# Performance work log

Measured on AMD Instinct MI355X. Metric: run time of the kernel, lower is better.

## Reference

```python
import jax, jax.numpy as jnp
import numpy as np
from jax import lax

T = 8
TAU = 2.0
ALPHA = 4.0   # spikingjelly surrogate.Sigmoid default alpha
EPS = 1e-5


def _kaiming(key, shape, fan_in):
    return jax.random.normal(key, shape, jnp.float32) * np.sqrt(2.0 / fan_in)


def setup_inputs() -> dict:
    key = jax.random.key(0)
    ks = jax.random.split(key, 16)
    d = {}
    d['x'] = jax.random.normal(ks[0], (128, 3, 32, 32), jnp.float32)
    convs = [('1', 32, 3), ('2', 32, 32), ('3', 64, 32), ('4', 64, 64), ('5', 128, 64), ('6', 128, 128)]
    for i, (s, co, ci) in enumerate(convs):
        d['w' + s] = _kaiming(ks[1 + i], (co, ci, 3, 3), ci * 9)
        d['b' + s] = jnp.zeros((co,), jnp.float32)
        d['g' + s] = jnp.ones((co,), jnp.float32)
        d['be' + s] = jnp.zeros((co,), jnp.float32)
    d['fc1_w'] = _kaiming(ks[7], (128, 2048), 2048)
    d['fc1_b'] = jnp.zeros((128,), jnp.float32)
    d['fc2_w'] = _kaiming(ks[8], (10, 128), 128)
    d['fc2_b'] = jnp.zeros((10,), jnp.float32)
    return d


def _conv2d(x, w, b):  # x [M,C,H,W], w [O,I,3,3], pad=1 stride=1
    y = lax.conv_general_dilated(x, w, (1, 1), ((1, 1), (1, 1)),
                                 dimension_numbers=('NCHW', 'OIHW', 'NCHW'))
    return y + b[None, :, None, None]


def _bn(x, g, be):  # training-mode BN over merged (T*N,H,W) batch
    m = x.mean(axis=(0, 2, 3))
    v = x.var(axis=(0, 2, 3))
    inv = g / jnp.sqrt(v + EPS)
    return x * inv[None, :, None, None] + (be - m * inv)[None, :, None, None]


def _lif(x_seq, th):
    # spikingjelly LIFNode defaults: decay_input=True, v_reset=0 (hard reset),
    # surrogate sigmoid gradient. x_seq: [T, ...]
    def step(v, x):
        v = v + (x - v) / TAU
        sig = jax.nn.sigmoid(ALPHA * (v - th))
        hard = (v >= th).astype(x.dtype)
        spike = lax.stop_gradient(hard - sig) + sig  # fwd: heaviside, bwd: sigmoid'
        return v * (1.0 - spike), spike
    return lax.scan(step, jnp.zeros_like(x_seq[0]), x_seq)[1]


def _maxpool(x):  # [M,C,H,W] -> 2x2 stride 2
    return lax.reduce_window(x, -jnp.inf, lax.max, (1, 1, 2, 2), (1, 1, 2, 2), 'VALID')


def _cbl(xs, w, b, g, be, th):  # conv-bn over merged TN, LIF scan over T
    t, n = xs.shape[0], xs.shape[1]
    m = xs.reshape((t * n,) + xs.shape[2:])
    y = _bn(_conv2d(m, w, b), g, be)
    return _lif(y.reshape((t, n) + y.shape[1:]), th)


def _pool_seq(xs):
    t, n = xs.shape[0], xs.shape[1]
    y = _maxpool(xs.reshape((t * n,) + xs.shape[2:]))
    return y.reshape((t, n) + y.shape[1:])


def _forward(x, w1, b1, g1, be1, w2, b2, g2, be2, w3, b3, g3, be3,
             w4, b4, g4, be4, w5, b5, g5, be5, w6, b6, g6, be6,
             fc1_w, fc1_b, fc2_w, fc2_b):
    th = 1.0
    xs = jnp.broadcast_to(x[None], (T,) + x.shape)  # [T,N,3,32,32]
    xs = _cbl(xs, w1, b1, g1, be1, th)
    xs = _cbl(xs, w2, b2, g2, be2, th)
    xs = _pool_seq(xs)                                # [T,N,32,16,16]
    xs = _cbl(xs, w3, b3, g3, be3, th)
    xs = _cbl(xs, w4, b4, g4, be4, th)
    xs = _pool_seq(xs)                                # [T,N,64,8,8]
    xs = _cbl(xs, w5, b5, g5, be5, th)
    xs = _cbl(xs, w6, b6, g6, be6, th)
    xs = _pool_seq(xs)                                # [T,N,128,4,4]
    t, n = xs.shape[0], xs.shape[1]
    f = xs.reshape(t, n, -1)                          # [T,N,2048]
    h = jnp.einsum('tnf,of->tno', f, fc1_w) + fc1_b
    h = _lif(h, 1.0)
    o = jnp.einsum('tnf,of->tno', h, fc2_w) + fc2_b
    o = _lif(o, 1.0)
    return o.mean(axis=0)                             # [N,10]


def reference(x, w1, b1, g1, be1, w2, b2, g2, be2, w3, b3, g3, be3,
              w4, b4, g4, be4, w5, b5, g5, be5, w6, b6, g6, be6,
              fc1_w, fc1_b, fc2_w, fc2_b):
    return _forward(x, w1, b1, g1, be1, w2, b2, g2, be2, w3, b3, g3, be3,
                    w4, b4, g4, be4, w5, b5, g5, be5, w6, b6, g6, be6,
                    fc1_w, fc1_b, fc2_w, fc2_b)
```

## Files before the change

### kernel.cpp

```cpp
#include <hip/hip_runtime.h>
#include <stdint.h>


#define T_STEPS 8
#define NBATCH 128

typedef __attribute__((ext_vector_type(8))) short short8;
typedef __attribute__((ext_vector_type(4))) float f32x4;

__device__ __forceinline__ uint16_t f2bf(float f) {
    uint32_t x = __float_as_uint(f);
    uint32_t r = x + 0x7FFFu + ((x >> 16) & 1u);
    return (uint16_t)(r >> 16);
}
__device__ __forceinline__ float bf2f(uint16_t h) {
    return __uint_as_float(((uint32_t)h) << 16);
}

__global__ void zero_kernel(float* p, int n) {
    int i = blockIdx.x * blockDim.x + threadIdx.x;
    if (i < n) p[i] = 0.0f;
}

__device__ __forceinline__ void tsplit(float v, uint16_t& h1, uint16_t& h2, uint16_t& h3) {
    h1 = f2bf(v);
    const float r1 = v - bf2f(h1);
    h2 = f2bf(r1);
    const float r2 = r1 - bf2f(h2);
    h3 = f2bf(r2);
}

__device__ __forceinline__ void prep_conv_one(const float* __restrict__ w,
                                              uint16_t* __restrict__ wp, int i, int CIN) {
    const int KC = CIN >> 5;
    const int sh = i % 9;
    const int ci = (i / 9) % CIN;
    const int co = i / (9 * CIN);
    uint16_t h1, h2, h3;
    tsplit(w[i], h1, h2, h3);
    uint16_t* base = wp + (size_t)((co >> 4) * KC + (ci >> 5)) * 14976
                        + sh * 1664 + (co & 15) * 104 + (ci & 31);
    base[0] = h1;
    base[32] = h2;
    base[64] = h3;
}

__device__ __forceinline__ void prep_fc1_one(const float* __restrict__ w,
                                             uint16_t* __restrict__ wp, int i) {
    const int kp = i & 2047;
    const int o = i >> 11;
    const int px = kp >> 7, c = kp & 127;
    uint16_t h1, h2, h3;
    tsplit(w[o * 2048 + c * 16 + px], h1, h2, h3);
    uint16_t* base = wp + (size_t)((o >> 4) * 64 + (kp >> 5)) * 1664
                        + (o & 15) * 104 + (kp & 31);
    base[0] = h1;
    base[32] = h2;
    base[64] = h3;
}

__global__ void prep_all_kernel(const float* __restrict__ W2, const float* __restrict__ W3,
                                const float* __restrict__ W4, const float* __restrict__ W5,
                                const float* __restrict__ W6, const float* __restrict__ F1,
                                uint16_t* __restrict__ P2, uint16_t* __restrict__ P3,
                                uint16_t* __restrict__ P4, uint16_t* __restrict__ P5,
                                uint16_t* __restrict__ P6, uint16_t* __restrict__ PF) {
    int i = blockIdx.x * blockDim.x + threadIdx.x;
    if (i < 9216) { prep_conv_one(W2, P2, i, 32); return; }
    i -= 9216;
    if (i < 18432) { prep_conv_one(W3, P3, i, 32); return; }
    i -= 18432;
    if (i < 36864) { prep_conv_one(W4, P4, i, 64); return; }
    i -= 36864;
    if (i < 73728) { prep_conv_one(W5, P5, i, 64); return; }
    i -= 73728;
    if (i < 147456) { prep_conv_one(W6, P6, i, 128); return; }
    i -= 147456;
    if (i < 262144) prep_fc1_one(F1, PF, i);
}

__global__ void border_all_kernel(uint8_t* S1, uint8_t* S2, uint8_t* S3,
                                  uint8_t* S4, uint8_t* S5, uint8_t* S6) {
    int i = blockIdx.x * blockDim.x + threadIdx.x;
    uint8_t* s;
    int C, HP, WPP;
    if (i < 1081344) { s = S1; C = 32; HP = 34; WPP = 34; }
    else if ((i -= 1081344) < 557056) { s = S2; C = 32; HP = 18; WPP = 18; }
    else if ((i -= 557056) < 1114112) { s = S3; C = 64; HP = 18; WPP = 18; }
    else if ((i -= 1114112) < 589824) { s = S4; C = 64; HP = 10; WPP = 10; }
    else if ((i -= 589824) < 1179648) { s = S5; C = 128; HP = 10; WPP = 10; }
    else if ((i -= 1179648) < 655360) { s = S6; C = 128; HP = 6; WPP = 6; }
    else return;
    const int C4 = C >> 2;
    const int NB = 2 * WPP + 2 * (HP - 2);
    const int c4 = i % C4;
    const int b = (i / C4) % NB;
    const int img = i / (C4 * NB);
    int py, px;
    if (b < WPP) { py = 0; px = b; }
    else if (b < 2 * WPP) { py = HP - 1; px = b - WPP; }
    else { const int r = b - 2 * WPP; py = 1 + (r >> 1); px = (r & 1) ? (WPP - 1) : 0; }
    *(uint32_t*)&s[(size_t)img * (HP * WPP * C) + (py * WPP + px) * C + 4 * c4] = 0u;
}

__global__ void conv3x3_kernel(const float* __restrict__ in,
                               const float* __restrict__ wgt,
                               const float* __restrict__ bias,
                               float* __restrict__ y,
                               float* __restrict__ ssum,
                               float* __restrict__ ssq,
                               int Cin, int H, int W) {
    const int m  = blockIdx.x;
    const int co = blockIdx.y;
    const int Cout = gridDim.y;
    const int HW = H * W;

    const float* wco = wgt + (size_t)co * Cin * 9;
    const float bv = bias[co];

    float lsum = 0.0f, lsq = 0.0f;

    for (int p = threadIdx.x; p < HW; p += blockDim.x) {
        const int hy = p / W;
        const int wx = p - hy * W;
        float acc = bv;
        for (int ci = 0; ci < Cin; ++ci) {
            const float* inc = in + ((size_t)m * Cin + ci) * HW;
            const float* wc = wco + ci * 9;
#pragma unroll
            for (int ky = 0; ky < 3; ++ky) {
                const int iy = hy + ky - 1;
                if (iy < 0 || iy >= H) continue;
#pragma unroll
                for (int kx = 0; kx < 3; ++kx) {
                    const int ix = wx + kx - 1;
                    if (ix < 0 || ix >= W) continue;
                    acc += inc[iy * W + ix] * wc[ky * 3 + kx];
                }
            }
        }
        y[((size_t)m * HW + p) * Cout + co] = acc;
        lsum += acc;
        lsq += acc * acc;
    }

    __shared__ float r1[256];
    __shared__ float r2[256];
    const int tid = threadIdx.x;
    r1[tid] = lsum;
    r2[tid] = lsq;
    __syncthreads();
    for (int s = blockDim.x >> 1; s > 0; s >>= 1) {
        if (tid < s) {
            r1[tid] += r1[tid + s];
            r2[tid] += r2[tid + s];
        }
        __syncthreads();
    }
    if (tid == 0) {
        atomicAdd(&ssum[co], r1[0]);
        atomicAdd(&ssq[co], r2[0]);
    }
}

template <int CIN, int COUT, int H, int W, int ROWS, int IMPB, int NCO, int KSPLIT>
__global__ __launch_bounds__(256) void conv_mfma_kernel(
    const uint8_t* __restrict__ in, const uint16_t* __restrict__ wp,
    const float* __restrict__ bias, float* __restrict__ y,
    float* __restrict__ ssum, float* __restrict__ ssq)
{
    constexpr int KC = CIN / 32;
    constexpr int WPP = W + 2;
    constexpr int HW = H * W;
    constexpr int PXU16 = CIN + 8;
    constexpr int ISTR_B = (H + 2) * WPP * CIN;
    constexpr int RB = H / ROWS;
    constexpr int NSTRIP = IMPB * ROWS * W / 16;
    constexpr int MSPLIT = 4 / KSPLIT;
    constexpr int SPW = NSTRIP / MSPLIT;
    constexpr int TILE_U16 = IMPB * (ROWS + 2) * WPP * PXU16;
    constexpr int TILE_B = IMPB * (ROWS + 2) * WPP * CIN;
    constexpr int NIT = KC * 9;
    constexpr int ITW = NIT / KSPLIT;
    constexpr int CS = NCO * 16 + 1;
    static_assert(IMPB == 1 || ROWS == H, "impb needs full-image tiles");
    static_assert(NSTRIP % MSPLIT == 0 && NSTRIP % 4 == 0, "strips");
    static_assert(NIT % KSPLIT == 0, "ksplit");
    static_assert(TILE_B % 16 == 0, "tile u8 16B");
    static_assert(KSPLIT == 1 || TILE_U16 * 2 >= NSTRIP * 16 * CS * 4, "C fits");

    __shared__ __align__(16) uint16_t sp[TILE_U16];
    __shared__ float bn[NCO * 32];

    const int tid = threadIdx.x;
    const int lane = tid & 63;
    const int wav = tid >> 6;
    const int kg = wav / MSPLIT;
    const int mg = wav - kg * MSPLIT;
    const int col = lane & 15;
    const int quad = lane >> 4;

    const int m0 = (blockIdx.x / RB) * IMPB;
    const int ybase = (blockIdx.x % RB) * ROWS;

    if (tid < NCO * 32) bn[tid] = 0.0f;

    {
        const uint8_t* src = in + (size_t)m0 * ISTR_B + (size_t)ybase * WPP * CIN;
        for (int i = tid; i < TILE_B / 16; i += 256) {
            const uint4 v = ((const uint4*)src)[i];
            const int b = i * 16;
            const int px = b / CIN;
            const int ci = b - px * CIN;
            uint32_t* d = (uint32_t*)&sp[px * PXU16 + ci];
            d[0] = ((v.x & 1u) | (((v.x >> 8) & 1u) << 16)) * 0x3F80u;
            d[1] = (((v.x >> 16) & 1u) | (((v.x >> 24) & 1u) << 16)) * 0x3F80u;
            d[2] = ((v.y & 1u) | (((v.y >> 8) & 1u) << 16)) * 0x3F80u;
            d[3] = (((v.y >> 16) & 1u) | (((v.y >> 24) & 1u) << 16)) * 0x3F80u;
            d[4] = ((v.z & 1u) | (((v.z >> 8) & 1u) << 16)) * 0x3F80u;
            d[5] = (((v.z >> 16) & 1u) | (((v.z >> 24) & 1u) << 16)) * 0x3F80u;
            d[6] = ((v.w & 1u) | (((v.w >> 8) & 1u) << 16)) * 0x3F80u;
            d[7] = (((v.w >> 16) & 1u) | (((v.w >> 24) & 1u) << 16)) * 0x3F80u;
        }
    }
    __syncthreads();

    int abase[SPW];
#pragma unroll
    for (int s = 0; s < SPW; ++s) {
        const int p = (mg * SPW + s) * 16 + col;
        const int img = p / (ROWS * W);
        const int rem = p % (ROWS * W);
        abase[s] = ((img * (ROWS + 2) + rem / W) * WPP + rem % W) * PXU16 + quad * 8;
    }

    f32x4 acc[SPW][NCO];
#pragma unroll
    for (int s = 0; s < SPW; ++s)
#pragma unroll
        for (int j = 0; j < NCO; ++j) acc[s][j] = (f32x4)0.0f;

    const uint16_t* wbase = wp + ((size_t)blockIdx.y * NCO * KC) * 14976
                               + col * 104 + quad * 8;

    auto loadB = [&](short8 (&buf)[NCO][3], int it) {
        const int kc = it / 9, sh = it - kc * 9;
#pragma unroll
        for (int j = 0; j < NCO; ++j) {
            const uint16_t* p = wbase + (size_t)(j * KC + kc) * 14976 + sh * 1664;
            buf[j][0] = *(const short8*)p;
            buf[j][1] = *(const short8*)(p + 32);
            buf[j][2] = *(const short8*)(p + 64);
        }
    };
    auto mfmaStep = [&](short8 (&buf)[NCO][3], int it) {
        const int kc = it / 9, sh = it - kc * 9;
        const int dy = sh / 3, dx = sh - dy * 3;
        const int shoff = (dy * WPP + dx) * PXU16 + kc * 32;
#pragma unroll
        for (int s = 0; s < SPW; ++s) {
            const short8 a = *(const short8*)&sp[abase[s] + shoff];
#pragma unroll
            for (int j = 0; j < NCO; ++j) {
                f32x4 t = acc[s][j];
                t = __builtin_amdgcn_mfma_f32_16x16x32_bf16(a, buf[j][0], t, 0, 0, 0);
                t = __builtin_amdgcn_mfma_f32_16x16x32_bf16(a, buf[j][1], t, 0, 0, 0);
                t = __builtin_amdgcn_mfma_f32_16x16x32_bf16(a, buf[j][2], t, 0, 0, 0);
                acc[s][j] = t;
            }
        }
    };

    short8 bufA[NCO][3], bufB[NCO][3];
    const int it0 = kg * ITW, it1 = it0 + ITW;
    loadB(bufA, it0);
    int it = it0;
#pragma unroll 1
    for (; it + 2 <= it1; it += 2) {
        loadB(bufB, it + 1);
        mfmaStep(bufA, it);
        if (it + 2 < it1) loadB(bufA, it + 2);
        mfmaStep(bufB, it + 1);
    }
    if (it < it1) mfmaStep(bufA, it);

    if constexpr (KSPLIT == 1) {
#pragma unroll
        for (int j = 0; j < NCO; ++j) {
            const int co0 = (blockIdx.y * NCO + j) * 16;
            const float bv = bias[co0 + col];
#pragma unroll
            for (int s = 0; s < SPW; ++s) {
                const int pb_ = (mg * SPW + s) * 16 + quad * 4;
                float sum = 0.0f, sq = 0.0f;
#pragma unroll
                for (int r = 0; r < 4; ++r) {
                    const float v = acc[s][j][r] + bv;
                    const int p = pb_ + r;
                    const int img = p / (ROWS * W);
                    const int pxim = p % (ROWS * W) + ybase * W;
                    y[((size_t)(m0 + img) * HW + pxim) * COUT + co0 + col] = v;
                    sum += v;
                    sq += v * v;
                }
                sum += __shfl_xor(sum, 16, 64);
                sum += __shfl_xor(sum, 32, 64);
                sq += __shfl_xor(sq, 16, 64);
                sq += __shfl_xor(sq, 32, 64);
                if (quad == 0) {
                    atomicAdd(&bn[j * 32 + col], sum);
                    atomicAdd(&bn[j * 32 + 16 + col], sq);
                }
            }
        }
    } else {
        float* Csh = (float*)sp;
        __syncthreads();
        if (kg == 0) {
#pragma unroll
            for (int s = 0; s < SPW; ++s)
#pragma unroll
                for (int j = 0; j < NCO; ++j)
#pragma unroll
                    for (int r = 0; r < 4; ++r)
                        Csh[((mg * SPW + s) * 16 + quad * 4 + r) * CS + j * 16 + col]
                            = acc[s][j][r];
        }
        __syncthreads();
#pragma unroll
        for (int k = 1; k < KSPLIT; ++k) {
            if (kg == k) {
#pragma unroll
                for (int s = 0; s < SPW; ++s)
#pragma unroll
                    for (int j = 0; j < NCO; ++j)
#pragma unroll
                        for (int r = 0; r < 4; ++r)
                            Csh[((mg * SPW + s) * 16 + quad * 4 + r) * CS + j * 16 + col]
                                += acc[s][j][r];
            }
            __syncthreads();
        }
        constexpr int ES = NSTRIP / 4;
#pragma unroll
        for (int s2 = 0; s2 < ES; ++s2) {
            const int gs = wav * ES + s2;
#pragma unroll
            for (int j = 0; j < NCO; ++j) {
                const int co0 = (blockIdx.y * NCO + j) * 16;
                const float bv = bias[co0 + col];
                float sum = 0.0f, sq = 0.0f;
#pragma unroll
                for (int r = 0; r < 4; ++r) {
                    const float v = Csh[(gs * 16 + quad * 4 + r) * CS + j * 16 + col] + bv;
                    const int p = gs * 16 + quad * 4 + r;
                    const int img = p / (ROWS * W);
                    const int pxim = p % (ROWS * W) + ybase * W;
                    y[((size_t)(m0 + img) * HW + pxim) * COUT + co0 + col] = v;
                    sum += v;
                    sq += v * v;
                }
                sum += __shfl_xor(sum, 16, 64);
                sum += __shfl_xor(sum, 32, 64);
                sq += __shfl_xor(sq, 16, 64);
                sq += __shfl_xor(sq, 32, 64);
                if (quad == 0) {
                    atomicAdd(&bn[j * 32 + col], sum);
                    atomicAdd(&bn[j * 32 + 16 + col], sq);
                }
            }
        }
    }
    __syncthreads();
    if (tid < NCO * 32) {
        const int j = tid >> 5, r = tid & 31;
        const int co0 = (blockIdx.y * NCO + j) * 16;
        if (r < 16) atomicAdd(&ssum[co0 + r], bn[j * 32 + r]);
        else atomicAdd(&ssq[co0 + r - 16], bn[j * 32 + r]);
    }
}

__global__ void bnlif1_pad_kernel(const float* __restrict__ y,
                                  const float* __restrict__ ssum,
                                  const float* __restrict__ ssq,
                                  const float* __restrict__ g,
                                  const float* __restrict__ be,
                                  uint8_t* __restrict__ s, float invM) {
    constexpr int OSTR = 34 * 34 * 32;
    const int i = blockIdx.x * blockDim.x + threadIdx.x;
    if (i >= NBATCH * 1024 * 8) return;
    const int c4 = i & 7;
    const int px = (i >> 3) & 1023;
    const int n = i >> 13;
    const int c0 = 4 * c4;
    float z[4], v[4];
    const float4 q = *(const float4*)&y[((size_t)n * 1024 + px) * 32 + c0];
    const float* qf = (const float*)&q;
#pragma unroll
    for (int c = 0; c < 4; ++c) {
        const float m = ssum[c0 + c] * invM;
        const float inv = g[c0 + c] / sqrtf(ssq[c0 + c] * invM - m * m + 1e-5f);
        z[c] = qf[c] * inv + (be[c0 + c] - m * inv);
        v[c] = 0.0f;
    }
    const int pyy = px >> 5, pxx = px & 31;
    const size_t obase = (size_t)n * OSTR + ((pyy + 1) * 34 + pxx + 1) * 32 + c0;
    const size_t ot = (size_t)NBATCH * OSTR;
#pragma unroll
    for (int t = 0; t < T_STEPS; ++t) {
        uint32_t pk = 0;
#pragma unroll
        for (int c = 0; c < 4; ++c) {
            v[c] += (z[c] - v[c]) * 0.5f;
            if (v[c] >= 1.0f) { v[c] = 0.0f; pk |= 1u << (8 * c); }
        }
        *(uint32_t*)&s[t * ot + obase] = pk;
    }
}

template <int C, int H, int W>
__global__ void bnlif_pad_kernel(const float* __restrict__ y,
                                 const float* __restrict__ ssum,
                                 const float* __restrict__ ssq,
                                 const float* __restrict__ g,
                                 const float* __restrict__ be,
                                 uint8_t* __restrict__ s, float invM) {
    constexpr int C4 = C / 4;
    constexpr int HW = H * W;
    constexpr int OSTR = (H + 2) * (W + 2) * C;
    const int i = blockIdx.x * blockDim.x + threadIdx.x;
    if (i >= NBATCH * HW * C4) return;
    const int c4 = i % C4;
    const int px = (i / C4) % HW;
    const int n = i / (C4 * HW);
    const int c0 = 4 * c4;
    float inv[4], sh[4], v[4];
#pragma unroll
    for (int c = 0; c < 4; ++c) {
        const float m = ssum[c0 + c] * invM;
        inv[c] = g[c0 + c] / sqrtf(ssq[c0 + c] * invM - m * m + 1e-5f);
        sh[c] = be[c0 + c] - m * inv[c];
        v[c] = 0.0f;
    }
    const size_t ybase = ((size_t)n * HW + px) * C + c0;
    const size_t tstride = (size_t)NBATCH * HW * C;
    const int pyy = px / W, pxx = px % W;
    const size_t obase = (size_t)n * OSTR + ((pyy + 1) * (W + 2) + pxx + 1) * C + c0;
    const size_t ot = (size_t)NBATCH * OSTR;
#pragma unroll
    for (int t = 0; t < T_STEPS; ++t) {
        const float4 q = *(const float4*)&y[t * tstride + ybase];
        const float* qf = (const float*)&q;
        uint32_t pk = 0;
#pragma unroll
        for (int c = 0; c < 4; ++c) {
            const float z = qf[c] * inv[c] + sh[c];
            v[c] += (z - v[c]) * 0.5f;
            if (v[c] >= 1.0f) { v[c] = 0.0f; pk |= 1u << (8 * c); }
        }
        *(uint32_t*)&s[t * ot + obase] = pk;
    }
}

template <int C, int H, int W>
__global__ void bnlifpool_pad_kernel(const float* __restrict__ y,
                                     const float* __restrict__ ssum,
                                     const float* __restrict__ ssq,
                                     const float* __restrict__ g,
                                     const float* __restrict__ be,
                                     uint8_t* __restrict__ s, float invM) {
    constexpr int C4 = C / 4;
    constexpr int PH = H / 2, PW = W / 2;
    constexpr int OSTR = (PH + 2) * (PW + 2) * C;
    const int i = blockIdx.x * blockDim.x + threadIdx.x;
    if (i >= NBATCH * PH * PW * C4) return;
    const int c4 = i % C4;
    const int pw = (i / C4) % PW;
    const int ph = (i / (C4 * PW)) % PH;
    const int n = i / (C4 * PW * PH);
    const int c0 = 4 * c4;
    float inv[4], sh[4], v[4][4];
#pragma unroll
    for (int c = 0; c < 4; ++c) {
        const float m = ssum[c0 + c] * invM;
        inv[c] = g[c0 + c] / sqrtf(ssq[c0 + c] * invM - m * m + 1e-5f);
        sh[c] = be[c0 + c] - m * inv[c];
#pragma unroll
        for (int p = 0; p < 4; ++p) v[p][c] = 0.0f;
    }
    const size_t base = (((size_t)n * H + 2 * ph) * W + 2 * pw) * C + c0;
    const size_t tstride = (size_t)NBATCH * H * W * C;
    const size_t obase = (size_t)n * OSTR + ((ph + 1) * (PW + 2) + pw + 1) * C + c0;
    const size_t ot = (size_t)NBATCH * OSTR;
#pragma unroll
    for (int t = 0; t < T_STEPS; ++t) {
        const float* yt = y + t * tstride + base;
        float4 q[4];
        q[0] = *(const float4*)&yt[0];
        q[1] = *(const float4*)&yt[C];
        q[2] = *(const float4*)&yt[(size_t)W * C];
        q[3] = *(const float4*)&yt[(size_t)W * C + C];
        uint32_t pk = 0;
#pragma unroll
        for (int p = 0; p < 4; ++p) {
            const float* qf = (const float*)&q[p];
#pragma unroll
            for (int c = 0; c < 4; ++c) {
                const float z = qf[c] * inv[c] + sh[c];
                v[p][c] += (z - v[p][c]) * 0.5f;
                if (v[p][c] >= 1.0f) { v[p][c] = 0.0f; pk |= 1u << (8 * c); }
            }
        }
        *(uint32_t*)&s[t * ot + obase] = pk;
    }
}

__global__ __launch_bounds__(256) void fc1_mfma_kernel(
    const uint8_t* __restrict__ f, const uint16_t* __restrict__ wfc,
    const float* __restrict__ b, float* __restrict__ h)
{
    __shared__ __align__(16) uint16_t A[16 * 2056];
    const int tid = threadIdx.x;
    const int lane = tid & 63, wav = tid >> 6;
    const int col = lane & 15, quad = lane >> 4;
    const int r0 = blockIdx.x * 16;

    {
        const int row = tid >> 4, px = tid & 15;
        const int py = px >> 2, pxx = px & 3;
        const uint8_t* src = f + (size_t)(r0 + row) * 4608
                             + ((py + 1) * 6 + pxx + 1) * 128;
        uint32_t* dst = (uint32_t*)&A[row * 2056 + px * 128];
#pragma unroll
        for (int i = 0; i < 8; ++i) {
            const uint4 v = ((const uint4*)src)[i];
            dst[8 * i + 0] = ((v.x & 1u) | (((v.x >> 8) & 1u) << 16)) * 0x3F80u;
            dst[8 * i + 1] = (((v.x >> 16) & 1u) | (((v.x >> 24) & 1u) << 16)) * 0x3F80u;
            dst[8 * i + 2] = ((v.y & 1u) | (((v.y >> 8) & 1u) << 16)) * 0x3F80u;
            dst[8 * i + 3] = (((v.y >> 16) & 1u) | (((v.y >> 24) & 1u) << 16)) * 0x3F80u;
            dst[8 * i + 4] = ((v.z & 1u) | (((v.z >> 8) & 1u) << 16)) * 0x3F80u;
            dst[8 * i + 5] = (((v.z >> 16) & 1u) | (((v.z >> 24) & 1u) << 16)) * 0x3F80u;
            dst[8 * i + 6] = ((v.w & 1u) | (((v.w >> 8) & 1u) << 16)) * 0x3F80u;
            dst[8 * i + 7] = (((v.w >> 16) & 1u) | (((v.w >> 24) & 1u) << 16)) * 0x3F80u;
        }
    }
    __syncthreads();

    const int coblk = blockIdx.y * 4 + wav;
    const uint16_t* wbase = wfc + (size_t)coblk * 64 * 1664 + col * 104 + quad * 8;
    f32x4 acc = (f32x4)0.0f;

    auto loadB = [&](short8 (&buf)[3], int kc) {
        const uint16_t* p = wbase + kc * 1664;
        buf[0] = *(const short8*)p;
        buf[1] = *(const short8*)(p + 32);
        buf[2] = *(const short8*)(p + 64);
    };
    auto step = [&](short8 (&buf)[3], int kc) {
        const short8 a = *(const short8*)&A[col * 2056 + kc * 32 + quad * 8];
        acc = __builtin_amdgcn_mfma_f32_16x16x32_bf16(a, buf[0], acc, 0, 0, 0);
        acc = __builtin_amdgcn_mfma_f32_16x16x32_bf16(a, buf[1], acc, 0, 0, 0);
        acc = __builtin_amdgcn_mfma_f32_16x16x32_bf16(a, buf[2], acc, 0, 0, 0);
    };

    short8 bA[3], bB[3];
    loadB(bA, 0);
#pragma unroll 1
    for (int kc = 0; kc + 2 <= 64; kc += 2) {
        loadB(bB, kc + 1);
        step(bA, kc);
        if (kc + 2 < 64) loadB(bA, kc + 2);
        step(bB, kc + 1);
    }

    const int o = coblk * 16 + col;
    const float bv = b[o];
#pragma unroll
    for (int r = 0; r < 4; ++r)
        h[(size_t)(r0 + quad * 4 + r) * 128 + o] = acc[r] + bv;
}

__global__ void lif_fc_kernel(const float* __restrict__ h,
                              uint8_t* __restrict__ s, int NF) {
    const int i = blockIdx.x * blockDim.x + threadIdx.x;
    if (i >= NF) return;
    float v = 0.0f;
#pragma unroll
    for (int t = 0; t < T_STEPS; ++t) {
        const float z = h[(size_t)t * NF + i];
        v += (z - v) * 0.5f;
        const float sp = (v >= 1.0f) ? 1.0f : 0.0f;
        s[(size_t)t * NF + i] = (uint8_t)sp;
        v *= (1.0f - sp);
    }
}

__global__ void fc2_kernel(const uint8_t* __restrict__ sh,
                           const float* __restrict__ w,
                           const float* __restrict__ b,
                           float* __restrict__ out) {
    const int i = blockIdx.x * blockDim.x + threadIdx.x;
    if (i >= NBATCH * 10) return;
    const int k = i % 10;
    const int n = i / 10;
    float v = 0.0f, acc = 0.0f;
    for (int t = 0; t < T_STEPS; ++t) {
        const uint8_t* row = sh + ((size_t)t * NBATCH + n) * 128;
        float z = b[k];
        for (int o = 0; o < 128; ++o)
            z += (float)row[o] * w[k * 128 + o];
        v += (z - v) * 0.5f;
        const float sp = (v >= 1.0f) ? 1.0f : 0.0f;
        acc += sp;
        v *= (1.0f - sp);
    }
    out[i] = acc * (1.0f / T_STEPS);
}

extern "C" void kernel_launch(void* const* d_in, const int* in_sizes, int n_in,
                              void* d_out, int out_size, void* d_ws, size_t ws_size,
                              hipStream_t stream) {
    const float* x   = (const float*)d_in[0];
    const float* W1  = (const float*)d_in[1];
    const float* Bi1 = (const float*)d_in[2];
    const float* G1  = (const float*)d_in[3];
    const float* BE1 = (const float*)d_in[4];
    const float* W2  = (const float*)d_in[5];
    const float* Bi2 = (const float*)d_in[6];
    const float* G2  = (const float*)d_in[7];
    const float* BE2 = (const float*)d_in[8];
    const float* W3  = (const float*)d_in[9];
    const float* Bi3 = (const float*)d_in[10];
    const float* G3  = (const float*)d_in[11];
    const float* BE3 = (const float*)d_in[12];
    const float* W4  = (const float*)d_in[13];
    const float* Bi4 = (const float*)d_in[14];
    const float* G4  = (const float*)d_in[15];
    const float* BE4 = (const float*)d_in[16];
    const float* W5  = (const float*)d_in[17];
    const float* Bi5 = (const float*)d_in[18];
    const float* G5  = (const float*)d_in[19];
    const float* BE5 = (const float*)d_in[20];
    const float* W6  = (const float*)d_in[21];
    const float* Bi6 = (const float*)d_in[22];
    const float* G6  = (const float*)d_in[23];
    const float* BE6 = (const float*)d_in[24];
    const float* FC1W = (const float*)d_in[25];
    const float* FC1B = (const float*)d_in[26];
    const float* FC2W = (const float*)d_in[27];
    const float* FC2B = (const float*)d_in[28];

    uint8_t* ws = (uint8_t*)d_ws;
    float*   Y  = (float*)ws;
    const size_t SOFF = 134217728;
    uint8_t* S1 = ws + SOFF;
    uint8_t* S2 = ws + SOFF;
    uint8_t* S3 = ws + SOFF + 10616832;
    uint8_t* S4 = ws + SOFF;
    uint8_t* S5 = ws + SOFF + 6553600;
    uint8_t* S6 = ws + SOFF + 19660800;
    float*   stats = (float*)(ws + SOFF + 37879808);
    float*   h     = (float*)(ws + SOFF + 37879808 + 8192);
    uint8_t* shb   = ws + SOFF + 37879808 + 8192 + 524288;
    uint16_t* Wp   = (uint16_t*)(shb + 131072);
    uint16_t* Wp2p = Wp;
    uint16_t* Wp3p = Wp + 29952;
    uint16_t* Wp4p = Wp + 89856;
    uint16_t* Wp5p = Wp + 209664;
    uint16_t* Wp6p = Wp + 449280;
    uint16_t* Wfc1 = Wp + 928512;

    zero_kernel<<<(1536 + 255) / 256, 256, 0, stream>>>(stats, 1536);
    prep_all_kernel<<<(547840 + 255) / 256, 256, 0, stream>>>(
        W2, W3, W4, W5, W6, FC1W, Wp2p, Wp3p, Wp4p, Wp5p, Wp6p, Wfc1);
    border_all_kernel<<<(5177344 + 255) / 256, 256, 0, stream>>>(S1, S2, S3, S4, S5, S6);

    const int TN = T_STEPS * NBATCH;

    {
        dim3 g(NBATCH, 32);
        conv3x3_kernel<<<g, 256, 0, stream>>>(x, W1, Bi1, Y,
                                              stats + 0, stats + 128, 3, 32, 32);
        bnlif1_pad_kernel<<<(NBATCH * 1024 * 8) / 256, 256, 0, stream>>>(
            Y, stats + 0, stats + 128, G1, BE1, S1, 1.0f / 131072.0f);
    }
    {
        conv_mfma_kernel<32, 32, 32, 32, 16, 1, 2, 1><<<dim3(TN * 2, 1), 256, 0, stream>>>(
            S1, Wp2p, Bi2, Y, stats + 256, stats + 384);
        bnlifpool_pad_kernel<32, 32, 32><<<(NBATCH * 16 * 16 * 8) / 256, 256, 0, stream>>>(
            Y, stats + 256, stats + 384, G2, BE2, S2, 1.0f / (1024.0f * 1024.0f));
    }
    {
        conv_mfma_kernel<32, 64, 16, 16, 16, 2, 2, 1><<<dim3(TN / 2, 2), 256, 0, stream>>>(
            S2, Wp3p, Bi3, Y, stats + 512, stats + 640);
        bnlif_pad_kernel<64, 16, 16><<<(NBATCH * 256 * 16) / 256, 256, 0, stream>>>(
            Y, stats + 512, stats + 640, G3, BE3, S3, 1.0f / (1024.0f * 256.0f));
    }
    {
        conv_mfma_kernel<64, 64, 16, 16, 16, 1, 2, 2><<<dim3(TN, 2), 256, 0, stream>>>(
            S3, Wp4p, Bi4, Y, stats + 768, stats + 896);
        bnlifpool_pad_kernel<64, 16, 16><<<(NBATCH * 8 * 8 * 16) / 256, 256, 0, stream>>>(
            Y, stats + 768, stats + 896, G4, BE4, S4, 1.0f / (1024.0f * 256.0f));
    }
    {
        conv_mfma_kernel<64, 128, 8, 8, 8, 2, 2, 2><<<dim3(TN / 2, 4), 256, 0, stream>>>(
            S4, Wp5p, Bi5, Y, stats + 1024, stats + 1152);
        bnlif_pad_kernel<128, 8, 8><<<(NBATCH * 64 * 32) / 256, 256, 0, stream>>>(
            Y, stats + 1024, stats + 1152, G5, BE5, S5, 1.0f / (1024.0f * 64.0f));
    }
    {
        conv_mfma_kernel<128, 128, 8, 8, 8, 2, 2, 4><<<dim3(TN / 2, 4), 256, 0, stream>>>(
            S5, Wp6p, Bi6, Y, stats + 1280, stats + 1408);
        bnlifpool_pad_kernel<128, 8, 8><<<(NBATCH * 4 * 4 * 32) / 256, 256, 0, stream>>>(
            Y, stats + 1280, stats + 1408, G6, BE6, S6, 1.0f / (1024.0f * 64.0f));
    }
    fc1_mfma_kernel<<<dim3(64, 2), 256, 0, stream>>>(S6, Wfc1, FC1B, h);
    lif_fc_kernel<<<(NBATCH * 128 + 255) / 256, 256, 0, stream>>>(h, shb, NBATCH * 128);
    fc2_kernel<<<(NBATCH * 10 + 255) / 256, 256, 0, stream>>>(shb, FC2W, FC2B, (float*)d_out);
}
```

Measured before the change: 691.7 us.

## Rewrite first conv with shared-memory input tile and register weights

Replaces the generic per-output-channel direct conv for the 3-channel first layer with a specialized kernel. Each block loads an 8-row input tile (with halo) into shared memory once, and each thread keeps its channel's 27 weights in registers. It computes 4 adjacent pixels per row from a register window, which makes the 32-channel output stores coalesced. Batch-norm statistics are reduced through shared-memory atomics instead of a tree reduction. The grid shrinks from 128x32 to 128x4 blocks, trading parallelism for input reuse across output channels.

```diff
diff --git a/kernel.cpp b/kernel.cpp
--- a/kernel.cpp
+++ b/kernel.cpp
@@ -103,64 +103,75 @@
     *(uint32_t*)&s[(size_t)img * (HP * WPP * C) + (py * WPP + px) * C + 4 * c4] = 0u;
 }
 
-__global__ void conv3x3_kernel(const float* __restrict__ in,
-                               const float* __restrict__ wgt,
-                               const float* __restrict__ bias,
-                               float* __restrict__ y,
-                               float* __restrict__ ssum,
-                               float* __restrict__ ssq,
-                               int Cin, int H, int W) {
-    const int m  = blockIdx.x;
-    const int co = blockIdx.y;
-    const int Cout = gridDim.y;
-    const int HW = H * W;
-
-    const float* wco = wgt + (size_t)co * Cin * 9;
+__global__ __launch_bounds__(256) void conv1_kernel(
+    const float* __restrict__ x, const float* __restrict__ w,
+    const float* __restrict__ bias, float* __restrict__ y,
+    float* __restrict__ ssum, float* __restrict__ ssq)
+{
+    __shared__ float tile[3][10][34];
+    __shared__ float bnl[64];
+    const int tid = threadIdx.x;
+    const int m = blockIdx.x;
+    const int y0 = blockIdx.y * 8;
+    const int co = tid & 31;
+    const int strip = tid >> 5;
+
+    if (tid < 64) bnl[tid] = 0.0f;
+    for (int i = tid; i < 3 * 10 * 34; i += 256) ((float*)tile)[i] = 0.0f;
+    __syncthreads();
+
+    {
+        const int gy0 = (y0 == 0) ? 0 : y0 - 1;
+        const int gy1 = (y0 + 8 > 31) ? 31 : y0 + 8;
+        const int nrows = gy1 - gy0 + 1;
+        for (int i = tid; i < 3 * nrows * 32; i += 256) {
+            const int gx = i & 31;
+            const int r = (i >> 5) % nrows;
+            const int ci = i / (32 * nrows);
+            const int gy = gy0 + r;
+            tile[ci][gy - y0 + 1][gx + 1] =
+                x[((size_t)m * 3 + ci) * 1024 + gy * 32 + gx];
+        }
+    }
+    __syncthreads();
+
+    float wr[27];
+#pragma unroll
+    for (int j = 0; j < 27; ++j) wr[j] = w[co * 27 + j];
     const float bv = bias[co];
 
     float lsum = 0.0f, lsq = 0.0f;
-
-    for (int p = threadIdx.x; p < HW; p += blockDim.x) {
-        const int hy = p / W;
-        const int wx = p - hy * W;
-        float acc = bv;
-        for (int ci = 0; ci < Cin; ++ci) {
-            const float* inc = in + ((size_t)m * Cin + ci) * HW;
-            const float* wc = wco + ci * 9;
-#pragma unroll
-            for (int ky = 0; ky < 3; ++ky) {
-                const int iy = hy + ky - 1;
-                if (iy < 0 || iy >= H) continue;
-#pragma unroll
-                for (int kx = 0; kx < 3; ++kx) {
-                    const int ix = wx + kx - 1;
-                    if (ix < 0 || ix >= W) continue;
-                    acc += inc[iy * W + ix] * wc[ky * 3 + kx];
-                }
-            }
-        }
-        y[((size_t)m * HW + p) * Cout + co] = acc;
-        lsum += acc;
-        lsq += acc * acc;
-    }
-
-    __shared__ float r1[256];
-    __shared__ float r2[256];
-    const int tid = threadIdx.x;
-    r1[tid] = lsum;
-    r2[tid] = lsq;
+#pragma unroll
+    for (int g = 0; g < 8; ++g) {
+        float s[3][3][6];
+#pragma unroll
+        for (int ci = 0; ci < 3; ++ci)
+#pragma unroll
+            for (int ky = 0; ky < 3; ++ky)
+#pragma unroll
+                for (int c = 0; c < 6; ++c)
+                    s[ci][ky][c] = tile[ci][g + ky][strip * 4 + c];
+#pragma unroll
+        for (int r = 0; r < 4; ++r) {
+            float acc = bv;
+#pragma unroll
+            for (int ci = 0; ci < 3; ++ci)
+#pragma unroll
+                for (int ky = 0; ky < 3; ++ky)
+#pragma unroll
+                    for (int kx = 0; kx < 3; ++kx)
+                        acc += s[ci][ky][r + kx] * wr[ci * 9 + ky * 3 + kx];
+            const int lx = strip * 4 + r;
+            y[(((size_t)m * 1024) + (y0 + g) * 32 + lx) * 32 + co] = acc;
+            lsum += acc;
+            lsq += acc * acc;
+        }
+    }
+    atomicAdd(&bnl[co], lsum);
+    atomicAdd(&bnl[32 + co], lsq);
     __syncthreads();
-    for (int s = blockDim.x >> 1; s > 0; s >>= 1) {
-        if (tid < s) {
-            r1[tid] += r1[tid + s];
-            r2[tid] += r2[tid + s];
-        }
-        __syncthreads();
-    }
-    if (tid == 0) {
-        atomicAdd(&ssum[co], r1[0]);
-        atomicAdd(&ssq[co], r2[0]);
-    }
+    if (tid < 32) atomicAdd(&ssum[tid], bnl[tid]);
+    else if (tid < 64) atomicAdd(&ssq[tid - 32], bnl[tid]);
 }
 
 template <int CIN, int COUT, int H, int W, int ROWS, int IMPB, int NCO, int KSPLIT>
@@ -678,9 +689,8 @@
     const int TN = T_STEPS * NBATCH;
 
     {
-        dim3 g(NBATCH, 32);
-        conv3x3_kernel<<<g, 256, 0, stream>>>(x, W1, Bi1, Y,
-                                              stats + 0, stats + 128, 3, 32, 32);
+        conv1_kernel<<<dim3(NBATCH, 4), 256, 0, stream>>>(x, W1, Bi1, Y,
+                                                          stats + 0, stats + 128);
         bnlif1_pad_kernel<<<(NBATCH * 1024 * 8) / 256, 256, 0, stream>>>(
             Y, stats + 0, stats + 128, G1, BE1, S1, 1.0f / 131072.0f);
     }
```

Measured after the change: 740.7 us. +7.1%, slower.
